# Kernel optimization log

Measured on AMD Instinct MI355X. Metric: run time of the kernel, lower is better.

Reference implementation:

```python
import jax, jax.numpy as jnp
import numpy as np

T, C, H, W = 16, 3, 512, 512
PS, PT = 7, 1
NQ = 262144


def setup_inputs() -> dict:
    key = jax.random.key(0)
    k1, k2, k3, k4 = jax.random.split(key, 4)
    vid2fill = jnp.zeros((T, C, H, W), jnp.float32)
    patches = jax.random.normal(k1, (NQ, PT, C, PS, PS), jnp.float32)
    # queryInds columns: (t, h, w) top-left corners, each kept in-bounds
    qt = jax.random.randint(k2, (NQ, 1), 0, T - PT + 1)
    qh = jax.random.randint(k3, (NQ, 1), 0, H - PS + 1)
    qw = jax.random.randint(k4, (NQ, 1), 0, W - PS + 1)
    queryInds = jnp.concatenate([qt, qh, qw], axis=1).astype(jnp.int32)
    return {"vid2fill": vid2fill, "patches": patches, "queryInds": queryInds}


def reference(vid2fill, patches, queryInds):
    # vid2fill: [T,C,H,W]; patches: [N,pt,C,ps,ps]; queryInds: [N,3] = (t,h,w)
    T_, C_, H_, W_ = vid2fill.shape
    N, pt, _, ps, _ = patches.shape
    ti = queryInds[:, 0, None] + jnp.arange(pt)  # [N,pt]
    hi = queryInds[:, 1, None] + jnp.arange(ps)  # [N,ps]
    wi = queryInds[:, 2, None] + jnp.arange(ps)  # [N,ps]
    # flat spatial-temporal index over (t,h,w): [N,pt,ps,ps]
    flat = (ti[:, :, None, None] * H_ + hi[:, None, :, None]) * W_ + wi[:, None, None, :]
    # channels-last flat video [T*H*W, C] for a single vectorized scatter-add
    vid_flat = vid2fill.transpose(0, 2, 3, 1).reshape(-1, C_)
    p = patches.transpose(0, 1, 3, 4, 2).reshape(-1, C_)  # [N*pt*ps*ps, C]
    out = vid_flat.at[flat.reshape(-1)].add(p)
    return out.reshape(T_, H_, W_, C_).transpose(0, 3, 1, 2)
```

## Files before the change

### kernel.cpp

```cpp
#include <hip/hip_runtime.h>

constexpr int T_ = 16, C_ = 3, H_ = 512, W_ = 512, PS_ = 7;
constexpr int PATCH_ELEMS = C_ * PS_ * PS_;
constexpr int TILE  = 32;
constexpr int HALO  = PS_ - 1;
constexpr int LTILE = TILE + HALO;
constexpr int LSTRIDE = 40;
constexpr int NTH = H_ / TILE, NTW = W_ / TILE;
constexpr int NBINS = T_ * NTH * NTW;
constexpr int LDS_PER_C  = LTILE * LSTRIDE;
constexpr int ACC_FLOATS = C_ * LDS_PER_C;
constexpr int INTERIOR   = C_ * TILE * TILE;
constexpr int HALO_A = HALO * LTILE;
constexpr int HALO_B = TILE * HALO;
constexpr int HALO_PER_C    = HALO_A + HALO_B;
constexpr int HALO_PER_TILE = C_ * HALO_PER_C;
constexpr int CAP = 160;
constexpr int BTHR = 192;
constexpr int BR = 8;
constexpr int SSLOT = 50;
constexpr int BAND = HALO * TILE + (TILE - HALO) * HALO;

constexpr size_t OFF_COUNTS = 0;
constexpr size_t OFF_LIST   = 16384;
constexpr size_t OFF_HALO   = OFF_LIST + (size_t)NBINS * CAP * 4;
constexpr size_t WS_NEEDED  = OFF_HALO + (size_t)NBINS * HALO_PER_TILE * 4;

typedef const __attribute__((address_space(1))) float* gas_fp;
typedef __attribute__((address_space(3))) float* las_fp;

__global__ void zero_counts_kernel(int* counts) {
    counts[blockIdx.x * 1024 + threadIdx.x] = 0;
}

__global__ void scatter_kernel(const int* __restrict__ q, int* __restrict__ counts,
                               int* __restrict__ list, int nq) {
    int n = blockIdx.x * 256 + threadIdx.x;
    if (n >= nq) return;
    int t = q[3 * n], h = q[3 * n + 1], w = q[3 * n + 2];
    int bin = (t * NTH + (h >> 5)) * NTW + (w >> 5);
    int pos = atomicAdd(counts + bin, 1);
    if (pos < CAP) list[bin * CAP + pos] = (n << 10) | ((h & 31) << 5) | (w & 31);
}

__global__ __launch_bounds__(BTHR, 4) void accum_kernel(
    const float* __restrict__ patches, const int* __restrict__ counts,
    const int* __restrict__ list, const float* __restrict__ vid,
    float* __restrict__ out, float* __restrict__ halo) {
    __shared__ float acc[ACC_FLOATS];
    __shared__ float stage[C_][2][BR * SSLOT];
    __shared__ int recs[CAP];
    const int bin = blockIdx.x;
    const int t = bin >> 8;
    const int h0 = ((bin >> 4) & 15) * TILE, w0 = (bin & 15) * TILE;
    const int tid = threadIdx.x;
    const int lane = tid & 63, wid = tid >> 6;

    for (int i = tid; i < ACC_FLOATS; i += BTHR) acc[i] = 0.f;
    int cnt = counts[bin];
    if (cnt > CAP) cnt = CAP;
    if (tid < cnt) recs[tid] = list[bin * CAP + tid];
    __syncthreads();

    {
        const int c = wid;
        const bool act = lane < PS_ * PS_;
        const int loff = act ? (lane / PS_) * LSTRIDE + (lane % PS_) : 0;
        float* __restrict__ ac = acc + c * LDS_PER_C;
        const int nb = (cnt + BR - 1) / BR;

        auto issue = [&](int bb, int u) {
            int base = bb * BR;
            if (act) {
#pragma unroll
                for (int j = 0; j < BR; ++j) {
                    int idx = base + j;
                    if (idx > cnt - 1) idx = cnt - 1;
                    int rr = recs[idx];
                    const float* g = patches + (size_t)(unsigned)(rr >> 10) * PATCH_ELEMS
                                     + c * (PS_ * PS_) + lane;
                    __builtin_amdgcn_global_load_lds(
                        (gas_fp)(const void*)g,
                        (las_fp)(void*)&stage[c][u][j * SSLOT], 4, 0, 0);
                }
            }
            __builtin_amdgcn_sched_barrier(0);
        };

        if (nb > 0) {
            issue(0, 0);
            issue(nb > 1 ? 1 : 0, 1);
            for (int b = 0; b < nb; ++b) {
                asm volatile("s_waitcnt vmcnt(8)" ::: "memory");
                __builtin_amdgcn_sched_barrier(0);
                const int base = b * BR;
                int lim = cnt - base; if (lim > BR) lim = BR;
                const float* sb = &stage[c][b & 1][0];
                for (int j = 0; j < lim; ++j) {
                    int rr = recs[base + j];
                    int bofs = ((rr >> 5) & 31) * LSTRIDE + (rr & 31) + loff;
                    if (act) ac[bofs] += sb[j * SSLOT + lane];
                }
                int nxt = b + 2; if (nxt > nb - 1) nxt = nb - 1;
                issue(nxt, b & 1);
            }
        }
    }
    __syncthreads();

    const size_t obase = (size_t)t * C_ * H_ * W_;
    for (int i = tid; i < INTERIOR / 4; i += BTHR) {
        int cc = i >> 8, rem = i & 255, y = rem >> 3, x4 = rem & 7;
        size_t g = obase + (size_t)cc * (H_ * W_) + (size_t)(h0 + y) * W_ + (w0 + x4 * 4);
        const float4 vv = *reinterpret_cast<const float4*>(vid + g);
        const float4 aa = *reinterpret_cast<const float4*>(
            &acc[cc * LDS_PER_C + y * LSTRIDE + x4 * 4]);
        float4 r; r.x = vv.x + aa.x; r.y = vv.y + aa.y; r.z = vv.z + aa.z; r.w = vv.w + aa.w;
        *reinterpret_cast<float4*>(out + g) = r;
    }
    float* hp = halo + (size_t)bin * HALO_PER_TILE;
    for (int i = tid; i < HALO_PER_TILE; i += BTHR) {
        int cc = i / HALO_PER_C, r = i % HALO_PER_C;
        int y, x;
        if (r < HALO_A) { y = TILE + r / LTILE; x = r % LTILE; }
        else            { int r2 = r - HALO_A; y = r2 / HALO; x = TILE + r2 % HALO; }
        hp[i] = acc[cc * LDS_PER_C + y * LSTRIDE + x];
    }
}

__global__ void halo_add_kernel(const float* __restrict__ halo,
                                float* __restrict__ out, int total) {
    int idx = blockIdx.x * 256 + threadIdx.x;
    if (idx >= total) return;
    int bin = idx / (C_ * BAND);
    int r = idx - bin * (C_ * BAND);
    int c = r / BAND;
    int s = r - c * BAND;
    int hm, wm;
    if (s < HALO * TILE) { hm = s >> 5; wm = s & 31; }
    else { int s2 = s - HALO * TILE; hm = HALO + s2 / HALO; wm = s2 - (s2 / HALO) * HALO; }
    int t = bin >> 8, i = (bin >> 4) & 15, j = bin & 15;
    bool top  = (hm < HALO) && (i > 0);
    bool left = (wm < HALO) && (j > 0);
    if (!(top || left)) return;
    float a = 0.f;
    if (top) {
        int tb = (t * NTH + (i - 1)) * NTW + j;
        a += halo[(size_t)tb * HALO_PER_TILE + c * HALO_PER_C + hm * LTILE + wm];
    }
    if (left) {
        int tb = (t * NTH + i) * NTW + (j - 1);
        a += halo[(size_t)tb * HALO_PER_TILE + c * HALO_PER_C + HALO_A + hm * HALO + wm];
    }
    if (top && left) {
        int tb = (t * NTH + (i - 1)) * NTW + (j - 1);
        a += halo[(size_t)tb * HALO_PER_TILE + c * HALO_PER_C + hm * LTILE + (TILE + wm)];
    }
    size_t g = (((size_t)t * C_ + c) * H_ + (i * TILE + hm)) * W_ + (j * TILE + wm);
    out[g] += a;
}

__global__ void scatter_add_kernel(const float* __restrict__ patches,
                                   const int* __restrict__ qinds,
                                   float* __restrict__ out, int total) {
    int tid = blockIdx.x * blockDim.x + threadIdx.x;
    if (tid >= total) return;
    int n = tid / PATCH_ELEMS;
    int r = tid - n * PATCH_ELEMS;
    int c = r / (PS_ * PS_);
    int rr = r - c * (PS_ * PS_);
    int ih = rr / PS_, iw = rr - ih * PS_;
    int t = qinds[n * 3 + 0], h = qinds[n * 3 + 1], w = qinds[n * 3 + 2];
    int out_idx = ((t * C_ + c) * H_ + (h + ih)) * W_ + (w + iw);
    atomicAdd(out + out_idx, patches[tid]);
}

extern "C" void kernel_launch(void* const* d_in, const int* in_sizes, int n_in,
                              void* d_out, int out_size, void* d_ws, size_t ws_size,
                              hipStream_t stream) {
    const float* vid     = (const float*)d_in[0];
    const float* patches = (const float*)d_in[1];
    const int*   qinds   = (const int*)d_in[2];
    float*       out     = (float*)d_out;
    const int nq = in_sizes[2] / 3;

    if (ws_size < WS_NEEDED) {
        hipMemcpyAsync(out, vid, (size_t)out_size * sizeof(float),
                       hipMemcpyDeviceToDevice, stream);
        int total = nq * PATCH_ELEMS;
        scatter_add_kernel<<<(total + 255) / 256, 256, 0, stream>>>(patches, qinds, out, total);
        return;
    }

    char* ws = (char*)d_ws;
    int*   counts = (int*)(ws + OFF_COUNTS);
    int*   list   = (int*)(ws + OFF_LIST);
    float* halo   = (float*)(ws + OFF_HALO);

    zero_counts_kernel<<<NBINS / 1024, 1024, 0, stream>>>(counts);
    scatter_kernel<<<(nq + 255) / 256, 256, 0, stream>>>(qinds, counts, list, nq);
    accum_kernel<<<NBINS, BTHR, 0, stream>>>(patches, counts, list, vid, out, halo);
    int total_band = NBINS * C_ * BAND;
    halo_add_kernel<<<(total_band + 255) / 256, 256, 0, stream>>>(halo, out, total_band);
}
```

Baseline: 330.5 us.

## Fuse binning, tile accumulation and halo fixup into one cooperative persistent kernel

Replaces the four-kernel pipeline (zero counts, bin queries, per-tile accumulate, halo add) with a single cooperative persistent kernel that uses grid-wide syncs between phases, sized from an occupancy query. The accumulate loop drops the global_load_lds double-buffered staging in favour of register-prefetched loads of eight patch rows per step, and occupancy hints rise from 4 to 6 blocks. This aims to remove kernel launch gaps and inter-kernel drain time. The cost is grid.sync overhead, persistent blocks looping over bins, and less explicit latency hiding on the patch gathers.

```diff
diff --git a/kernel.cpp b/kernel.cpp
--- a/kernel.cpp
+++ b/kernel.cpp
@@ -1,4 +1,7 @@
 #include <hip/hip_runtime.h>
+#include <hip/hip_cooperative_groups.h>
+
+namespace cg = cooperative_groups;
 
 constexpr int T_ = 16, C_ = 3, H_ = 512, W_ = 512, PS_ = 7;
 constexpr int PATCH_ELEMS = C_ * PS_ * PS_;
@@ -17,8 +20,6 @@
 constexpr int HALO_PER_TILE = C_ * HALO_PER_C;
 constexpr int CAP = 160;
 constexpr int BTHR = 192;
-constexpr int BR = 8;
-constexpr int SSLOT = 50;
 constexpr int BAND = HALO * TILE + (TILE - HALO) * HALO;
 
 constexpr size_t OFF_COUNTS = 0;
@@ -26,8 +27,137 @@
 constexpr size_t OFF_HALO   = OFF_LIST + (size_t)NBINS * CAP * 4;
 constexpr size_t WS_NEEDED  = OFF_HALO + (size_t)NBINS * HALO_PER_TILE * 4;
 
-typedef const __attribute__((address_space(1))) float* gas_fp;
-typedef __attribute__((address_space(3))) float* las_fp;
+__global__ __launch_bounds__(BTHR, 6) void fused_kernel(
+    const float* __restrict__ vid, const float* __restrict__ patches,
+    const int* __restrict__ qinds, float* __restrict__ out,
+    int* __restrict__ counts, int* __restrict__ list,
+    float* __restrict__ halo, int nq) {
+    cg::grid_group grid = cg::this_grid();
+    __shared__ float acc[ACC_FLOATS];
+    __shared__ int recs[CAP];
+    const int tid = threadIdx.x;
+    const int lane = tid & 63, wid = tid >> 6;
+    const int gsize = gridDim.x * BTHR;
+    const int gtid = blockIdx.x * BTHR + tid;
+
+    for (int i = gtid; i < NBINS; i += gsize) counts[i] = 0;
+    grid.sync();
+
+    for (int n = gtid; n < nq; n += gsize) {
+        int t = qinds[3 * n], h = qinds[3 * n + 1], w = qinds[3 * n + 2];
+        int bin = (t * NTH + (h >> 5)) * NTW + (w >> 5);
+        int pos = atomicAdd(counts + bin, 1);
+        if (pos < CAP) list[bin * CAP + pos] = (n << 10) | ((h & 31) << 5) | (w & 31);
+    }
+    grid.sync();
+
+    for (int bin = blockIdx.x; bin < NBINS; bin += gridDim.x) {
+        const int t = bin >> 8;
+        const int h0 = ((bin >> 4) & 15) * TILE, w0 = (bin & 15) * TILE;
+        for (int i = tid; i < ACC_FLOATS; i += BTHR) acc[i] = 0.f;
+        int cnt = counts[bin];
+        if (cnt > CAP) cnt = CAP;
+        if (tid < cnt) recs[tid] = list[bin * CAP + tid];
+        __syncthreads();
+        {
+            const int c = wid;
+            const bool act = lane < PS_ * PS_;
+            const int loff = act ? (lane / PS_) * LSTRIDE + (lane % PS_) : 0;
+            float* __restrict__ ac = acc + c * LDS_PER_C;
+            const float* __restrict__ pc = patches + c * (PS_ * PS_);
+
+            float v0=0,v1=0,v2=0,v3=0,v4=0,v5=0,v6=0,v7=0;
+            int o0=0,o1=0,o2=0,o3=0,o4=0,o5=0,o6=0,o7=0;
+#define LDR(vv,oo,ii) { int rr = recs[(ii)]; \
+            oo = ((rr >> 5) & 31) * LSTRIDE + (rr & 31) + loff; \
+            vv = act ? pc[(size_t)(unsigned)(rr >> 10) * PATCH_ELEMS + lane] : 0.f; }
+            if (0 < cnt) LDR(v0,o0, 0)
+            if (1 < cnt) LDR(v1,o1, 1)
+            if (2 < cnt) LDR(v2,o2, 2)
+            if (3 < cnt) LDR(v3,o3, 3)
+            if (4 < cnt) LDR(v4,o4, 4)
+            if (5 < cnt) LDR(v5,o5, 5)
+            if (6 < cnt) LDR(v6,o6, 6)
+            if (7 < cnt) LDR(v7,o7, 7)
+            for (int p = 0; p < cnt; p += 8) {
+                float x0=v0,x1=v1,x2=v2,x3=v3,x4=v4,x5=v5,x6=v6,x7=v7;
+                int q0=o0,q1=o1,q2=o2,q3=o3,q4=o4,q5=o5,q6=o6,q7=o7;
+                int qq = p + 8;
+                if (qq     < cnt) LDR(v0,o0, qq)
+                if (qq + 1 < cnt) LDR(v1,o1, qq+1)
+                if (qq + 2 < cnt) LDR(v2,o2, qq+2)
+                if (qq + 3 < cnt) LDR(v3,o3, qq+3)
+                if (qq + 4 < cnt) LDR(v4,o4, qq+4)
+                if (qq + 5 < cnt) LDR(v5,o5, qq+5)
+                if (qq + 6 < cnt) LDR(v6,o6, qq+6)
+                if (qq + 7 < cnt) LDR(v7,o7, qq+7)
+                if (act) {
+                    ac[q0] += x0;
+                    if (p + 1 < cnt) ac[q1] += x1;
+                    if (p + 2 < cnt) ac[q2] += x2;
+                    if (p + 3 < cnt) ac[q3] += x3;
+                    if (p + 4 < cnt) ac[q4] += x4;
+                    if (p + 5 < cnt) ac[q5] += x5;
+                    if (p + 6 < cnt) ac[q6] += x6;
+                    if (p + 7 < cnt) ac[q7] += x7;
+                }
+            }
+#undef LDR
+        }
+        __syncthreads();
+
+        const size_t obase = (size_t)t * C_ * H_ * W_;
+        for (int i = tid; i < INTERIOR / 4; i += BTHR) {
+            int cc = i >> 8, rem = i & 255, y = rem >> 3, x4 = rem & 7;
+            size_t g = obase + (size_t)cc * (H_ * W_) + (size_t)(h0 + y) * W_ + (w0 + x4 * 4);
+            const float4 vv = *reinterpret_cast<const float4*>(vid + g);
+            const float4 aa = *reinterpret_cast<const float4*>(
+                &acc[cc * LDS_PER_C + y * LSTRIDE + x4 * 4]);
+            float4 r; r.x = vv.x + aa.x; r.y = vv.y + aa.y; r.z = vv.z + aa.z; r.w = vv.w + aa.w;
+            *reinterpret_cast<float4*>(out + g) = r;
+        }
+        float* hp = halo + (size_t)bin * HALO_PER_TILE;
+        for (int i = tid; i < HALO_PER_TILE; i += BTHR) {
+            int cc = i / HALO_PER_C, r = i % HALO_PER_C;
+            int y, x;
+            if (r < HALO_A) { y = TILE + r / LTILE; x = r % LTILE; }
+            else            { int r2 = r - HALO_A; y = r2 / HALO; x = TILE + r2 % HALO; }
+            hp[i] = acc[cc * LDS_PER_C + y * LSTRIDE + x];
+        }
+        __syncthreads();
+    }
+    grid.sync();
+
+    const int totalb = NBINS * C_ * BAND;
+    for (int idx = gtid; idx < totalb; idx += gsize) {
+        int bin = idx / (C_ * BAND);
+        int r = idx - bin * (C_ * BAND);
+        int c = r / BAND;
+        int s = r - c * BAND;
+        int hm, wm;
+        if (s < HALO * TILE) { hm = s >> 5; wm = s & 31; }
+        else { int s2 = s - HALO * TILE; hm = HALO + s2 / HALO; wm = s2 - (s2 / HALO) * HALO; }
+        int t = bin >> 8, i = (bin >> 4) & 15, j = bin & 15;
+        bool top  = (hm < HALO) && (i > 0);
+        bool left = (wm < HALO) && (j > 0);
+        if (!(top || left)) continue;
+        float a = 0.f;
+        if (top) {
+            int tb = (t * NTH + (i - 1)) * NTW + j;
+            a += halo[(size_t)tb * HALO_PER_TILE + c * HALO_PER_C + hm * LTILE + wm];
+        }
+        if (left) {
+            int tb = (t * NTH + i) * NTW + (j - 1);
+            a += halo[(size_t)tb * HALO_PER_TILE + c * HALO_PER_C + HALO_A + hm * HALO + wm];
+        }
+        if (top && left) {
+            int tb = (t * NTH + (i - 1)) * NTW + (j - 1);
+            a += halo[(size_t)tb * HALO_PER_TILE + c * HALO_PER_C + hm * LTILE + (TILE + wm)];
+        }
+        size_t g = (((size_t)t * C_ + c) * H_ + (i * TILE + hm)) * W_ + (j * TILE + wm);
+        out[g] += a;
+    }
+}
 
 __global__ void zero_counts_kernel(int* counts) {
     counts[blockIdx.x * 1024 + threadIdx.x] = 0;
@@ -43,12 +173,11 @@
     if (pos < CAP) list[bin * CAP + pos] = (n << 10) | ((h & 31) << 5) | (w & 31);
 }
 
-__global__ __launch_bounds__(BTHR, 4) void accum_kernel(
+__global__ __launch_bounds__(BTHR, 6) void accum_kernel(
     const float* __restrict__ patches, const int* __restrict__ counts,
     const int* __restrict__ list, const float* __restrict__ vid,
     float* __restrict__ out, float* __restrict__ halo) {
     __shared__ float acc[ACC_FLOATS];
-    __shared__ float stage[C_][2][BR * SSLOT];
     __shared__ int recs[CAP];
     const int bin = blockIdx.x;
     const int t = bin >> 8;
@@ -61,53 +190,20 @@
     if (cnt > CAP) cnt = CAP;
     if (tid < cnt) recs[tid] = list[bin * CAP + tid];
     __syncthreads();
-
     {
         const int c = wid;
         const bool act = lane < PS_ * PS_;
         const int loff = act ? (lane / PS_) * LSTRIDE + (lane % PS_) : 0;
         float* __restrict__ ac = acc + c * LDS_PER_C;
-        const int nb = (cnt + BR - 1) / BR;
-
-        auto issue = [&](int bb, int u) {
-            int base = bb * BR;
-            if (act) {
-#pragma unroll
-                for (int j = 0; j < BR; ++j) {
-                    int idx = base + j;
-                    if (idx > cnt - 1) idx = cnt - 1;
-                    int rr = recs[idx];
-                    const float* g = patches + (size_t)(unsigned)(rr >> 10) * PATCH_ELEMS
-                                     + c * (PS_ * PS_) + lane;
-                    __builtin_amdgcn_global_load_lds(
-                        (gas_fp)(const void*)g,
-                        (las_fp)(void*)&stage[c][u][j * SSLOT], 4, 0, 0);
-                }
-            }
-            __builtin_amdgcn_sched_barrier(0);
-        };
-
-        if (nb > 0) {
-            issue(0, 0);
-            issue(nb > 1 ? 1 : 0, 1);
-            for (int b = 0; b < nb; ++b) {
-                asm volatile("s_waitcnt vmcnt(8)" ::: "memory");
-                __builtin_amdgcn_sched_barrier(0);
-                const int base = b * BR;
-                int lim = cnt - base; if (lim > BR) lim = BR;
-                const float* sb = &stage[c][b & 1][0];
-                for (int j = 0; j < lim; ++j) {
-                    int rr = recs[base + j];
-                    int bofs = ((rr >> 5) & 31) * LSTRIDE + (rr & 31) + loff;
-                    if (act) ac[bofs] += sb[j * SSLOT + lane];
-                }
-                int nxt = b + 2; if (nxt > nb - 1) nxt = nb - 1;
-                issue(nxt, b & 1);
-            }
+        const float* __restrict__ pc = patches + c * (PS_ * PS_);
+        for (int p = 0; p < cnt; ++p) {
+            int rr = recs[p];
+            int o = ((rr >> 5) & 31) * LSTRIDE + (rr & 31) + loff;
+            float v = act ? pc[(size_t)(unsigned)(rr >> 10) * PATCH_ELEMS + lane] : 0.f;
+            if (act) ac[o] += v;
         }
     }
     __syncthreads();
-
     const size_t obase = (size_t)t * C_ * H_ * W_;
     for (int i = tid; i < INTERIOR / 4; i += BTHR) {
         int cc = i >> 8, rem = i & 255, y = rem >> 3, x4 = rem & 7;
@@ -197,6 +293,22 @@
     int*   list   = (int*)(ws + OFF_LIST);
     float* halo   = (float*)(ws + OFF_HALO);
 
+    static int maxb = -1;
+    if (maxb < 0) {
+        hipError_t oe = hipOccupancyMaxActiveBlocksPerMultiprocessor(
+            &maxb, fused_kernel, BTHR, 0);
+        if (oe != hipSuccess || maxb < 1) maxb = 0;
+    }
+    if (maxb > 0) {
+        int grid = 256 * maxb;
+        if (grid > NBINS) grid = NBINS;
+        void* args[] = {(void*)&vid, (void*)&patches, (void*)&qinds, (void*)&out,
+                        (void*)&counts, (void*)&list, (void*)&halo, (void*)&nq};
+        hipError_t e = hipLaunchCooperativeKernel((void*)fused_kernel, dim3(grid),
+                                                  dim3(BTHR), args, 0, stream);
+        if (e == hipSuccess) return;
+    }
+
     zero_counts_kernel<<<NBINS / 1024, 1024, 0, stream>>>(counts);
     scatter_kernel<<<(nq + 255) / 256, 256, 0, stream>>>(qinds, counts, list, nq);
     accum_kernel<<<NBINS, BTHR, 0, stream>>>(patches, counts, list, vid, out, halo);
```

New measurement: 700.0 us. 2.12x slower.
